# Kernel optimization log

Measured on AMD Instinct MI355X. Metric: run time of the kernel, lower is better.

## Reference

```python
import jax, jax.numpy as jnp
import numpy as np

N = 100000
E = 1600000
E_PAIR = 100000
D_IN = 128
D_H = 128


def _sage_mean(x, src, dst, W_neigh, W_self, b):
    # DGL SAGEConv('mean'): out = fc_self(h_dst) + fc_neigh(mean_{u in N(v)} h_u) + bias
    n = x.shape[0]
    msg_sum = jax.ops.segment_sum(x[src], dst, num_segments=n)          # [N, d]
    deg = jax.ops.segment_sum(jnp.ones(src.shape, x.dtype), dst, num_segments=n)
    h_neigh = msg_sum / jnp.maximum(deg, 1.0)[:, None]
    return x @ W_self.T + h_neigh @ W_neigh.T + b


def setup_inputs() -> dict:
    key = jax.random.key(0)
    ks = jax.random.split(key, 16)
    def lin(k, fan_out, fan_in):
        s = 1.0 / np.sqrt(fan_in)
        return jax.random.uniform(k, (fan_out, fan_in), jnp.float32, -s, s)
    inp = {
        'x': jax.random.normal(ks[0], (N, D_IN), jnp.float32),
        'edge_src': jax.random.randint(ks[1], (E,), 0, N),
        'edge_dst': jax.random.randint(ks[2], (E,), 0, N),
        'pos_src': jax.random.randint(ks[3], (E_PAIR,), 0, N),
        'pos_dst': jax.random.randint(ks[4], (E_PAIR,), 0, N),
        'neg_src': jax.random.randint(ks[5], (E_PAIR,), 0, N),
        'neg_dst': jax.random.randint(ks[6], (E_PAIR,), 0, N),
        # SAGEConv layer 1 (in_feats -> n_hidden)
        'W1_neigh': lin(ks[7], D_H, D_IN),
        'W1_self': lin(ks[8], D_H, D_IN),
        'b1': jnp.zeros((D_H,), jnp.float32),
        # SAGEConv layer 2 (n_hidden -> n_hidden)
        'W2_neigh': lin(ks[9], D_H, D_H),
        'W2_self': lin(ks[10], D_H, D_H),
        'b2': jnp.zeros((D_H,), jnp.float32),
        # predictor MLP: Linear(2h->h) ReLU Linear(h->h) ReLU Linear(h->1)
        'P1_w': lin(ks[11], D_H, 2 * D_H),
        'P1_b': jnp.zeros((D_H,), jnp.float32),
        'P2_w': lin(ks[12], D_H, D_H),
        'P2_b': jnp.zeros((D_H,), jnp.float32),
        'P3_w': lin(ks[13], 1, D_H),
        'P3_b': jnp.zeros((1,), jnp.float32),
    }
    return inp


def _predict(h_src, h_dst, P1_w, P1_b, P2_w, P2_b, P3_w, P3_b):
    h = jnp.concatenate([h_src, h_dst], axis=1)
    h = jax.nn.relu(h @ P1_w.T + P1_b)
    h = jax.nn.relu(h @ P2_w.T + P2_b)
    return h @ P3_w.T + P3_b


def reference(x, edge_src, edge_dst, pos_src, pos_dst, neg_src, neg_dst,
              W1_neigh, W1_self, b1, W2_neigh, W2_self, b2,
              P1_w, P1_b, P2_w, P2_b, P3_w, P3_b):
    h = _sage_mean(x, edge_src, edge_dst, W1_neigh, W1_self, b1)
    h = jax.nn.relu(h)
    h = _sage_mean(h, edge_src, edge_dst, W2_neigh, W2_self, b2)
    h_pos = _predict(h[pos_src], h[pos_dst], P1_w, P1_b, P2_w, P2_b, P3_w, P3_b)
    h_neg = _predict(h[neg_src], h[neg_dst], P1_w, P1_b, P2_w, P2_b, P3_w, P3_b)
    return (h_pos, h_neg)
```

## Files before the change

kernel.cpp:

```cpp
#include <hip/hip_runtime.h>
#include <hip/hip_bf16.h>
#include <hip/hip_fp16.h>


#define D 128
#define NR 512
#define PART_CHUNK 4096
#define LDA 40
#define LDC 264

typedef _Float16 f16x8 __attribute__((ext_vector_type(8)));
typedef float f32x4 __attribute__((ext_vector_type(4)));

__global__ __launch_bounds__(256) void k_regcount(
    const int* __restrict__ dst, int* __restrict__ region_cnt, int e, int bound) {
    __shared__ int s[NR];
    for (int i = threadIdx.x; i < NR; i += 256) s[i] = 0;
    __syncthreads();
    for (int i = blockIdx.x * 256 + threadIdx.x; i < e; i += gridDim.x * 256)
        atomicAdd(&s[dst[i] / bound], 1);
    __syncthreads();
    for (int i = threadIdx.x; i < NR; i += 256)
        if (s[i]) atomicAdd(&region_cnt[i], s[i]);
}

__global__ void k_regbase(const int* __restrict__ region_cnt,
                          int* __restrict__ region_base, int* __restrict__ region_cursor) {
    if (threadIdx.x == 0 && blockIdx.x == 0) {
        int run = 0;
        for (int r = 0; r < NR; ++r) {
            region_base[r] = run; region_cursor[r] = run; run += region_cnt[r];
        }
        region_base[NR] = run;
    }
}

__global__ __launch_bounds__(256) void k_regpart(
    const int* __restrict__ src, const int* __restrict__ dst,
    unsigned int* __restrict__ eout, int* __restrict__ region_cursor, int e, int bound) {
    __shared__ int s_cnt[NR];
    __shared__ int s_base[NR];
    for (int c0 = blockIdx.x * PART_CHUNK; c0 < e; c0 += gridDim.x * PART_CHUNK) {
        int cend = min(c0 + PART_CHUNK, e);
        for (int i = threadIdx.x; i < NR; i += 256) s_cnt[i] = 0;
        __syncthreads();
        for (int i = c0 + threadIdx.x; i < cend; i += 256)
            atomicAdd(&s_cnt[dst[i] / bound], 1);
        __syncthreads();
        for (int i = threadIdx.x; i < NR; i += 256)
            s_base[i] = s_cnt[i] ? atomicAdd(&region_cursor[i], s_cnt[i]) : 0;
        __syncthreads();
        for (int i = threadIdx.x; i < NR; i += 256) s_cnt[i] = 0;
        __syncthreads();
        for (int i = c0 + threadIdx.x; i < cend; i += 256) {
            int d = dst[i];
            int r = d / bound;
            unsigned int doff = (unsigned int)(d - r * bound);
            int p = atomicAdd(&s_cnt[r], 1);
            eout[s_base[r] + p] = (unsigned int)src[i] | (doff << 20);
        }
        __syncthreads();
    }
}

__global__ __launch_bounds__(256) void k_rowoff(
    const unsigned int* __restrict__ ep, const int* __restrict__ region_base,
    int* __restrict__ row_off, int n, int bound) {
    int r = blockIdx.x;
    int rlo = r * bound;
    if (threadIdx.x == 0 && r == 0) row_off[n] = region_base[NR];
    if (rlo >= n) return;
    int nn = min(bound, n - rlo);
    __shared__ int s_deg[256];
    __shared__ int s_scan[256];
    if (threadIdx.x < 256) s_deg[threadIdx.x] = 0;
    __syncthreads();
    int beg = region_base[r], end = region_base[r + 1];
    for (int i = beg + threadIdx.x; i < end; i += 256)
        atomicAdd(&s_deg[ep[i] >> 20], 1);
    __syncthreads();
    int v = (threadIdx.x < nn) ? s_deg[threadIdx.x] : 0;
    s_scan[threadIdx.x] = v;
    __syncthreads();
    #pragma unroll
    for (int off = 1; off < 256; off <<= 1) {
        int add = (threadIdx.x >= off) ? s_scan[threadIdx.x - off] : 0;
        __syncthreads();
        s_scan[threadIdx.x] += add;
        __syncthreads();
    }
    if (threadIdx.x < nn)
        row_off[rlo + threadIdx.x] = region_base[r] +
            (threadIdx.x ? s_scan[threadIdx.x - 1] : 0);
}

__global__ __launch_bounds__(256) void k_scatter3(
    const unsigned int* __restrict__ ep, const int* __restrict__ region_base,
    const int* __restrict__ row_off, int* __restrict__ csr, int n, int bound) {
    int r = blockIdx.x;
    int rlo = r * bound;
    if (rlo >= n) return;
    int nn = min(bound, n - rlo);
    __shared__ int s_cur[256];
    __shared__ int s_ro[256];
    if (threadIdx.x < nn) {
        s_cur[threadIdx.x] = 0;
        s_ro[threadIdx.x] = row_off[rlo + threadIdx.x];
    }
    __syncthreads();
    int beg = region_base[r], end = region_base[r + 1];
    for (int i = beg + threadIdx.x; i < end; i += 256) {
        unsigned int v = ep[i];
        int doff = v >> 20;
        int srcn = v & 0xFFFFF;
        int p = atomicAdd(&s_cur[doff], 1);
        csr[s_ro[doff] + p] = srcn;
    }
}

__global__ void k_cvt_f16(const float* __restrict__ src, _Float16* __restrict__ dst, int n8) {
    int i = blockIdx.x * 256 + threadIdx.x;
    if (i >= n8) return;
    const float4* s4 = (const float4*)src;
    float4 a = s4[2 * i], b = s4[2 * i + 1];
    f16x8 h;
    h[0] = (_Float16)a.x; h[1] = (_Float16)a.y; h[2] = (_Float16)a.z; h[3] = (_Float16)a.w;
    h[4] = (_Float16)b.x; h[5] = (_Float16)b.y; h[6] = (_Float16)b.z; h[7] = (_Float16)b.w;
    *(f16x8*)(dst + 8 * i) = h;
}

__global__ void k_cvt_weights(
    const float* __restrict__ W1s, const float* __restrict__ W1n,
    const float* __restrict__ W2s, const float* __restrict__ W2n,
    const float* __restrict__ P1w, const float* __restrict__ P2w,
    _Float16* __restrict__ Ws1f, _Float16* __restrict__ Wn1f,
    _Float16* __restrict__ Ws2f, _Float16* __restrict__ Wn2f,
    _Float16* __restrict__ P1wf, _Float16* __restrict__ P2wf) {
    int g = blockIdx.x * 256 + threadIdx.x;
    const float* src; _Float16* dst; int off;
    if      (g <  2048) { src = W1s; dst = Ws1f; off = g; }
    else if (g <  4096) { src = W1n; dst = Wn1f; off = g - 2048; }
    else if (g <  6144) { src = W2s; dst = Ws2f; off = g - 4096; }
    else if (g <  8192) { src = W2n; dst = Wn2f; off = g - 6144; }
    else if (g < 12288) { src = P1w; dst = P1wf; off = g - 8192; }
    else if (g < 14336) { src = P2w; dst = P2wf; off = g - 12288; }
    else return;
    const float4* s4 = (const float4*)src;
    float4 a = s4[2 * off], b = s4[2 * off + 1];
    f16x8 h;
    h[0] = (_Float16)a.x; h[1] = (_Float16)a.y; h[2] = (_Float16)a.z; h[3] = (_Float16)a.w;
    h[4] = (_Float16)b.x; h[5] = (_Float16)b.y; h[6] = (_Float16)b.z; h[7] = (_Float16)b.w;
    *(f16x8*)(dst + 8 * off) = h;
}

__global__ __launch_bounds__(256) void k_agg(
    const _Float16* __restrict__ Xf, const int* __restrict__ row_off,
    const int* __restrict__ csr, _Float16* __restrict__ Aggf, int n_nodes) {
    int g = blockIdx.x * 16 + (threadIdx.x >> 4);
    if (g >= n_nodes) return;
    int l = threadIdx.x & 15;
    int beg = row_off[g], end = row_off[g + 1];
    float acc[8] = {0.f, 0.f, 0.f, 0.f, 0.f, 0.f, 0.f, 0.f};
    int i = beg;
    for (; i + 4 <= end; i += 4) {
        int s0 = csr[i], s1 = csr[i + 1], s2 = csr[i + 2], s3 = csr[i + 3];
        f16x8 v0 = *(const f16x8*)(Xf + (size_t)s0 * D + l * 8);
        f16x8 v1 = *(const f16x8*)(Xf + (size_t)s1 * D + l * 8);
        f16x8 v2 = *(const f16x8*)(Xf + (size_t)s2 * D + l * 8);
        f16x8 v3 = *(const f16x8*)(Xf + (size_t)s3 * D + l * 8);
        #pragma unroll
        for (int j = 0; j < 8; ++j)
            acc[j] += ((float)v0[j] + (float)v1[j]) + ((float)v2[j] + (float)v3[j]);
    }
    for (; i < end; ++i) {
        int s0 = csr[i];
        f16x8 v0 = *(const f16x8*)(Xf + (size_t)s0 * D + l * 8);
        #pragma unroll
        for (int j = 0; j < 8; ++j) acc[j] += (float)v0[j];
    }
    float inv = 1.0f / fmaxf((float)(end - beg), 1.0f);
    f16x8 o;
    #pragma unroll
    for (int j = 0; j < 8; ++j) o[j] = (_Float16)(acc[j] * inv);
    *(f16x8*)(Aggf + (size_t)g * D + l * 8) = o;
}

__global__ __launch_bounds__(512) void k_transform(
    const _Float16* __restrict__ Xf, const _Float16* __restrict__ Aggf,
    const _Float16* __restrict__ Wsf, const _Float16* __restrict__ Wnf,
    const float* __restrict__ bias, _Float16* __restrict__ outf,
    int n_rows, int do_relu) {
    __shared__ _Float16 s_a[2][128 * LDA];
    __shared__ _Float16 s_b[2][128 * LDA];
    int tid = threadIdx.x;
    int w = tid >> 6, l = tid & 63;
    int wr = w >> 1, wc = w & 1;
    int l15 = l & 15, lk = l >> 4;
    int n0 = blockIdx.x * 128;
    int r = tid >> 2, q = tid & 3;
    int rstage = n0 + r; if (rstage >= n_rows) rstage = n_rows - 1;

    f32x4 acc[2][4];
    #pragma unroll
    for (int i = 0; i < 2; ++i)
        #pragma unroll
        for (int j = 0; j < 4; ++j) acc[i][j] = (f32x4){0.f, 0.f, 0.f, 0.f};

    int a_off = (wr * 32 + l15) * LDA + lk * 8;
    int b_off = (wc * 64 + l15) * LDA + lk * 8;
    int st_off = r * LDA + q * 8;

    {
        f16x8 av = *(const f16x8*)(Xf + (size_t)rstage * D + q * 8);
        f16x8 wv = *(const f16x8*)(Wsf + (size_t)r * D + q * 8);
        *(f16x8*)(&s_a[0][st_off]) = av;
        *(f16x8*)(&s_b[0][st_off]) = wv;
    }
    __syncthreads();

    for (int c = 0; c < 8; ++c) {
        int b = c & 1;
        f16x8 av, wv;
        if (c < 7) {
            int cn = c + 1;
            const _Float16* asrc = (cn < 4) ? Xf : Aggf;
            const _Float16* wsrc = (cn < 4) ? Wsf : Wnf;
            int kb = (cn & 3) * 32;
            av = *(const f16x8*)(asrc + (size_t)rstage * D + kb + q * 8);
            wv = *(const f16x8*)(wsrc + (size_t)r * D + kb + q * 8);
        }
        f16x8 af[2], bf[4];
        af[0] = *(const f16x8*)(&s_a[b][a_off]);
        af[1] = *(const f16x8*)(&s_a[b][a_off + 16 * LDA]);
        #pragma unroll
        for (int j = 0; j < 4; ++j) bf[j] = *(const f16x8*)(&s_b[b][b_off + j * 16 * LDA]);
        #pragma unroll
        for (int i = 0; i < 2; ++i)
            #pragma unroll
            for (int j = 0; j < 4; ++j)
                acc[i][j] = __builtin_amdgcn_mfma_f32_16x16x32_f16(af[i], bf[j], acc[i][j], 0, 0, 0);
        if (c < 7) {
            *(f16x8*)(&s_a[b ^ 1][st_off]) = av;
            *(f16x8*)(&s_b[b ^ 1][st_off]) = wv;
        }
        __syncthreads();
    }

    #pragma unroll
    for (int j = 0; j < 4; ++j) {
        int col = wc * 64 + j * 16 + l15;
        float bv = bias[col];
        #pragma unroll
        for (int i = 0; i < 2; ++i) {
            int rowb = n0 + wr * 32 + i * 16 + lk * 4;
            #pragma unroll
            for (int v = 0; v < 4; ++v) {
                int row = rowb + v;
                if (row < n_rows) {
                    float xv = acc[i][j][v] + bv;
                    if (do_relu) xv = fmaxf(xv, 0.f);
                    outf[(size_t)row * D + col] = (_Float16)xv;
                }
            }
        }
    }
}

__global__ __launch_bounds__(256) void k_mlp(
    const _Float16* __restrict__ Hf,
    const int* __restrict__ pos_src, const int* __restrict__ pos_dst,
    const int* __restrict__ neg_src, const int* __restrict__ neg_dst,
    const _Float16* __restrict__ P1wf, const float* __restrict__ P1b,
    const _Float16* __restrict__ P2wf, const float* __restrict__ P2b,
    const float* __restrict__ P3w, const float* __restrict__ P3b,
    float* __restrict__ out, int EP) {
    __shared__ _Float16 s_cat[64 * LDC];
    __shared__ _Float16 s_b[2][128 * LDA];
    __shared__ float s_red[64 * 2];
    __shared__ int s_node[128];
    int tid = threadIdx.x;
    int w = tid >> 6, l = tid & 63;
    int wr = w >> 1, wc = w & 1;
    int l15 = l & 15, lk = l >> 4;
    int p0 = blockIdx.x * 64;
    int twoEP = 2 * EP;

    if (tid < 128) {
        int p = p0 + (tid & 63);
        if (p >= twoEP) p = twoEP - 1;
        int node;
        if (tid < 64) node = (p < EP) ? pos_src[p] : neg_src[p - EP];
        else          node = (p < EP) ? pos_dst[p] : neg_dst[p - EP];
        s_node[tid] = node;
    }
    __syncthreads();

    #pragma unroll
    for (int e = 0; e < 8; ++e) {
        int idx = tid + e * 256;
        int rr = idx >> 4, u = idx & 15;
        int node = s_node[rr];
        f16x8 v = *(const f16x8*)(Hf + (size_t)node * D + u * 8);
        *(f16x8*)(s_cat + (rr & 63) * LDC + (rr >> 6) * 128 + u * 8) = v;
    }
    #pragma unroll
    for (int e = 0; e < 2; ++e) {
        int idx = tid + e * 256;
        int o = idx >> 2, q = idx & 3;
        *(f16x8*)(&s_b[0][o * LDA + q * 8]) = *(const f16x8*)(P1wf + (size_t)o * 256 + q * 8);
    }
    __syncthreads();

    f32x4 acc[2][4];
    #pragma unroll
    for (int i = 0; i < 2; ++i)
        #pragma unroll
        for (int j = 0; j < 4; ++j) acc[i][j] = (f32x4){0.f, 0.f, 0.f, 0.f};

    for (int c = 0; c < 8; ++c) {
        int b = c & 1;
        f16x8 nw[2];
        if (c < 7) {
            #pragma unroll
            for (int e = 0; e < 2; ++e) {
                int idx = tid + e * 256;
                int o = idx >> 2, q = idx & 3;
                nw[e] = *(const f16x8*)(P1wf + (size_t)o * 256 + (c + 1) * 32 + q * 8);
            }
        }
        f16x8 af[2], bf[4];
        af[0] = *(const f16x8*)(s_cat + (wr * 32 + l15) * LDC + c * 32 + lk * 8);
        af[1] = *(const f16x8*)(s_cat + (wr * 32 + 16 + l15) * LDC + c * 32 + lk * 8);
        #pragma unroll
        for (int j = 0; j < 4; ++j)
            bf[j] = *(const f16x8*)(&s_b[b][(wc * 64 + j * 16 + l15) * LDA + lk * 8]);
        #pragma unroll
        for (int i = 0; i < 2; ++i)
            #pragma unroll
            for (int j = 0; j < 4; ++j)
                acc[i][j] = __builtin_amdgcn_mfma_f32_16x16x32_f16(af[i], bf[j], acc[i][j], 0, 0, 0);
        if (c < 7) {
            #pragma unroll
            for (int e = 0; e < 2; ++e) {
                int idx = tid + e * 256;
                int o = idx >> 2, q = idx & 3;
                *(f16x8*)(&s_b[b ^ 1][o * LDA + q * 8]) = nw[e];
            }
        }
        __syncthreads();
    }

    #pragma unroll
    for (int j = 0; j < 4; ++j) {
        int col = wc * 64 + j * 16 + l15;
        float bv = P1b[col];
        #pragma unroll
        for (int i = 0; i < 2; ++i) {
            int rowb = wr * 32 + i * 16 + lk * 4;
            #pragma unroll
            for (int v = 0; v < 4; ++v)
                s_cat[(rowb + v) * LDC + col] = (_Float16)fmaxf(acc[i][j][v] + bv, 0.f);
        }
    }
    #pragma unroll
    for (int e = 0; e < 2; ++e) {
        int idx = tid + e * 256;
        int o = idx >> 2, q = idx & 3;
        *(f16x8*)(&s_b[0][o * LDA + q * 8]) = *(const f16x8*)(P2wf + (size_t)o * D + q * 8);
    }
    __syncthreads();

    f32x4 acc2[2][4];
    #pragma unroll
    for (int i = 0; i < 2; ++i)
        #pragma unroll
        for (int j = 0; j < 4; ++j) acc2[i][j] = (f32x4){0.f, 0.f, 0.f, 0.f};

    for (int c = 0; c < 4; ++c) {
        int b = c & 1;
        f16x8 nw[2];
        if (c < 3) {
            #pragma unroll
            for (int e = 0; e < 2; ++e) {
                int idx = tid + e * 256;
                int o = idx >> 2, q = idx & 3;
                nw[e] = *(const f16x8*)(P2wf + (size_t)o * D + (c + 1) * 32 + q * 8);
            }
        }
        f16x8 af[2], bf[4];
        af[0] = *(const f16x8*)(s_cat + (wr * 32 + l15) * LDC + c * 32 + lk * 8);
        af[1] = *(const f16x8*)(s_cat + (wr * 32 + 16 + l15) * LDC + c * 32 + lk * 8);
        #pragma unroll
        for (int j = 0; j < 4; ++j)
            bf[j] = *(const f16x8*)(&s_b[b][(wc * 64 + j * 16 + l15) * LDA + lk * 8]);
        #pragma unroll
        for (int i = 0; i < 2; ++i)
            #pragma unroll
            for (int j = 0; j < 4; ++j)
                acc2[i][j] = __builtin_amdgcn_mfma_f32_16x16x32_f16(af[i], bf[j], acc2[i][j], 0, 0, 0);
        if (c < 3) {
            #pragma unroll
            for (int e = 0; e < 2; ++e) {
                int idx = tid + e * 256;
                int o = idx >> 2, q = idx & 3;
                *(f16x8*)(&s_b[b ^ 1][o * LDA + q * 8]) = nw[e];
            }
        }
        __syncthreads();
    }

    float b2v[4], pw[4];
    #pragma unroll
    for (int j = 0; j < 4; ++j) {
        int col = wc * 64 + j * 16 + l15;
        b2v[j] = P2b[col];
        pw[j] = P3w[col];
    }
    #pragma unroll
    for (int i = 0; i < 2; ++i) {
        #pragma unroll
        for (int v = 0; v < 4; ++v) {
            float s = 0.f;
            #pragma unroll
            for (int j = 0; j < 4; ++j)
                s += fmaxf(acc2[i][j][v] + b2v[j], 0.f) * pw[j];
            s += __shfl_xor(s, 1);
            s += __shfl_xor(s, 2);
            s += __shfl_xor(s, 4);
            s += __shfl_xor(s, 8);
            if (l15 == 0)
                s_red[(wr * 32 + i * 16 + lk * 4 + v) * 2 + wc] = s;
        }
    }
    __syncthreads();
    if (tid < 64) {
        int p = p0 + tid;
        if (p < twoEP) out[p] = s_red[tid * 2] + s_red[tid * 2 + 1] + P3b[0];
    }
}

static inline size_t align_up(size_t x, size_t a) { return (x + a - 1) & ~(a - 1); }

extern "C" void kernel_launch(void* const* d_in, const int* in_sizes, int n_in,
                              void* d_out, int out_size, void* d_ws, size_t ws_size,
                              hipStream_t stream) {
    const float* x        = (const float*)d_in[0];
    const int*   edge_src = (const int*)d_in[1];
    const int*   edge_dst = (const int*)d_in[2];
    const int*   pos_src  = (const int*)d_in[3];
    const int*   pos_dst  = (const int*)d_in[4];
    const int*   neg_src  = (const int*)d_in[5];
    const int*   neg_dst  = (const int*)d_in[6];
    const float* W1n = (const float*)d_in[7];
    const float* W1s = (const float*)d_in[8];
    const float* b1  = (const float*)d_in[9];
    const float* W2n = (const float*)d_in[10];
    const float* W2s = (const float*)d_in[11];
    const float* b2  = (const float*)d_in[12];
    const float* P1w = (const float*)d_in[13];
    const float* P1b = (const float*)d_in[14];
    const float* P2w = (const float*)d_in[15];
    const float* P2b = (const float*)d_in[16];
    const float* P3w = (const float*)d_in[17];
    const float* P3b = (const float*)d_in[18];
    float* out = (float*)d_out;

    const int N = in_sizes[0] / D;
    const int E = in_sizes[1];
    const int EP = in_sizes[3];
    const int bound = (N + NR - 1) / NR;

    char* ws = (char*)d_ws;
    size_t off = 0;
    int* row_off = (int*)(ws + off); off = align_up(off + (size_t)(N + 1) * 4, 256);
    int* regmeta = (int*)(ws + off); off = align_up(off + (size_t)(3 * NR + 8) * 4, 256);
    int* csr     = (int*)(ws + off); off = align_up(off + (size_t)E * 4, 256);
    unsigned int* epart = (unsigned int*)(ws + off); off = align_up(off + (size_t)E * 4, 256);
    _Float16* xf   = (_Float16*)(ws + off); off = align_up(off + (size_t)N * D * 2, 256);
    _Float16* aggf = (_Float16*)(ws + off); off = align_up(off + (size_t)N * D * 2, 256);
    _Float16* h1f  = (_Float16*)(ws + off); off = align_up(off + (size_t)N * D * 2, 256);
    _Float16* h2f  = (_Float16*)(ws + off); off = align_up(off + (size_t)N * D * 2, 256);
    _Float16* Ws1f = (_Float16*)(ws + off); off = align_up(off + (size_t)D * D * 2, 256);
    _Float16* Wn1f = (_Float16*)(ws + off); off = align_up(off + (size_t)D * D * 2, 256);
    _Float16* Ws2f = (_Float16*)(ws + off); off = align_up(off + (size_t)D * D * 2, 256);
    _Float16* Wn2f = (_Float16*)(ws + off); off = align_up(off + (size_t)D * D * 2, 256);
    _Float16* P1wf = (_Float16*)(ws + off); off = align_up(off + (size_t)2 * D * D * 2, 256);
    _Float16* P2wf = (_Float16*)(ws + off); off = align_up(off + (size_t)D * D * 2, 256);
    (void)ws_size;

    int* region_cnt    = regmeta;
    int* region_base   = regmeta + NR;
    int* region_cursor = regmeta + 2 * NR + 4;

    hipMemsetAsync(region_cnt, 0, NR * 4, stream);
    k_regcount<<<128, 256, 0, stream>>>(edge_dst, region_cnt, E, bound);
    k_regbase<<<1, 1, 0, stream>>>(region_cnt, region_base, region_cursor);
    k_regpart<<<(E + PART_CHUNK - 1) / PART_CHUNK, 256, 0, stream>>>(
        edge_src, edge_dst, epart, region_cursor, E, bound);
    k_rowoff<<<NR, 256, 0, stream>>>(epart, region_base, row_off, N, bound);
    k_scatter3<<<NR, 256, 0, stream>>>(epart, region_base, row_off, csr, N, bound);

    k_cvt_f16<<<(N * D / 8 + 255) / 256, 256, 0, stream>>>(x, xf, N * D / 8);
    k_cvt_weights<<<56, 256, 0, stream>>>(W1s, W1n, W2s, W2n, P1w, P2w,
                                          Ws1f, Wn1f, Ws2f, Wn2f, P1wf, P2wf);

    const int ngrid = (N + 127) / 128;
    const int pgrid = (2 * EP + 63) / 64;

    k_agg<<<(N + 15) / 16, 256, 0, stream>>>(xf, row_off, csr, aggf, N);
    k_transform<<<ngrid, 512, 0, stream>>>(xf, aggf, Ws1f, Wn1f, b1, h1f, N, 1);
    k_agg<<<(N + 15) / 16, 256, 0, stream>>>(h1f, row_off, csr, aggf, N);
    k_transform<<<ngrid, 512, 0, stream>>>(h1f, aggf, Ws2f, Wn2f, b2, h2f, N, 0);

    k_mlp<<<pgrid, 256, 0, stream>>>(h2f, pos_src, pos_dst, neg_src, neg_dst,
                                     P1wf, P1b, P2wf, P2b, P3w, P3b, out, EP);
}
```

Before: 326.4 us.

## Precompute per-node predictor first-layer projections before gathering edge pairs

Splits the first predictor linear layer into source and destination halves and applies each once per node in a new GEMM kernel, k_pre. That kernel writes an N×256 half-precision table, which reuses the xf buffer and spills into the adjacent aggf buffer. The pair MLP then gathers the two precomputed halves, adds the bias and applies ReLU, which removes the per-pair 256-wide GEMM. It trades roughly half the first-layer FLOPs for an extra kernel launch and a large intermediate that must be written and then gathered.

```diff
diff --git a/kernel.cpp b/kernel.cpp
--- a/kernel.cpp
+++ b/kernel.cpp
@@ -7,7 +7,7 @@
 #define NR 512
 #define PART_CHUNK 4096
 #define LDA 40
-#define LDC 264
+#define LDH2 136
 
 typedef _Float16 f16x8 __attribute__((ext_vector_type(8)));
 typedef float f32x4 __attribute__((ext_vector_type(4)));
@@ -135,16 +135,26 @@
     const float* __restrict__ P1w, const float* __restrict__ P2w,
     _Float16* __restrict__ Ws1f, _Float16* __restrict__ Wn1f,
     _Float16* __restrict__ Ws2f, _Float16* __restrict__ Wn2f,
-    _Float16* __restrict__ P1wf, _Float16* __restrict__ P2wf) {
+    _Float16* __restrict__ P1cf, _Float16* __restrict__ P2wf) {
     int g = blockIdx.x * 256 + threadIdx.x;
+    if (g >= 14336) return;
     const float* src; _Float16* dst; int off;
+    if (g >= 8192 && g < 12288) {
+        int u = g - 8192;
+        int o = u >> 4, col = (u & 15) * 8;
+        src = P1w + (size_t)(o & 127) * 256 + ((o >> 7) * 128) + col;
+        float4 a = *(const float4*)src, b = *(const float4*)(src + 4);
+        f16x8 h;
+        h[0] = (_Float16)a.x; h[1] = (_Float16)a.y; h[2] = (_Float16)a.z; h[3] = (_Float16)a.w;
+        h[4] = (_Float16)b.x; h[5] = (_Float16)b.y; h[6] = (_Float16)b.z; h[7] = (_Float16)b.w;
+        *(f16x8*)(P1cf + (size_t)u * 8) = h;
+        return;
+    }
     if      (g <  2048) { src = W1s; dst = Ws1f; off = g; }
     else if (g <  4096) { src = W1n; dst = Wn1f; off = g - 2048; }
     else if (g <  6144) { src = W2s; dst = Ws2f; off = g - 4096; }
     else if (g <  8192) { src = W2n; dst = Wn2f; off = g - 6144; }
-    else if (g < 12288) { src = P1w; dst = P1wf; off = g - 8192; }
-    else if (g < 14336) { src = P2w; dst = P2wf; off = g - 12288; }
-    else return;
+    else                { src = P2w; dst = P2wf; off = g - 12288; }
     const float4* s4 = (const float4*)src;
     float4 a = s4[2 * off], b = s4[2 * off + 1];
     f16x8 h;
@@ -266,15 +276,80 @@
     }
 }
 
+__global__ __launch_bounds__(512) void k_pre(
+    const _Float16* __restrict__ Hf, const _Float16* __restrict__ P1cf,
+    _Float16* __restrict__ Pre, int n_rows) {
+    __shared__ _Float16 s_a[64 * LDA];
+    __shared__ _Float16 s_b[256 * LDA];
+    int tid = threadIdx.x;
+    int w = tid >> 6, l = tid & 63;
+    int wr = w >> 2, wc = w & 3;
+    int l15 = l & 15, lk = l >> 4;
+    int n0 = blockIdx.x * 64;
+
+    f32x4 acc[2][4];
+    #pragma unroll
+    for (int i = 0; i < 2; ++i)
+        #pragma unroll
+        for (int j = 0; j < 4; ++j) acc[i][j] = (f32x4){0.f, 0.f, 0.f, 0.f};
+
+    int a_off = (wr * 32 + l15) * LDA + lk * 8;
+
+    for (int c = 0; c < 4; ++c) {
+        int kb = c * 32;
+        __syncthreads();
+        if (tid < 256) {
+            int r = tid >> 2, q = tid & 3;
+            int rstage = n0 + r; if (rstage >= n_rows) rstage = n_rows - 1;
+            *(f16x8*)(&s_a[r * LDA + q * 8]) =
+                *(const f16x8*)(Hf + (size_t)rstage * D + kb + q * 8);
+        }
+        #pragma unroll
+        for (int e = 0; e < 2; ++e) {
+            int idx = tid + e * 512;
+            int o = idx >> 2, q = idx & 3;
+            *(f16x8*)(&s_b[o * LDA + q * 8]) =
+                *(const f16x8*)(P1cf + (size_t)o * 128 + kb + q * 8);
+        }
+        __syncthreads();
+        f16x8 af[2], bf[4];
+        af[0] = *(const f16x8*)(&s_a[a_off]);
+        af[1] = *(const f16x8*)(&s_a[a_off + 16 * LDA]);
+        #pragma unroll
+        for (int j = 0; j < 4; ++j)
+            bf[j] = *(const f16x8*)(&s_b[(wc * 64 + j * 16 + l15) * LDA + lk * 8]);
+        #pragma unroll
+        for (int i = 0; i < 2; ++i)
+            #pragma unroll
+            for (int j = 0; j < 4; ++j)
+                acc[i][j] = __builtin_amdgcn_mfma_f32_16x16x32_f16(af[i], bf[j], acc[i][j], 0, 0, 0);
+    }
+
+    #pragma unroll
+    for (int j = 0; j < 4; ++j) {
+        int col = wc * 64 + j * 16 + l15;
+        #pragma unroll
+        for (int i = 0; i < 2; ++i) {
+            int rowb = n0 + wr * 32 + i * 16 + lk * 4;
+            #pragma unroll
+            for (int v = 0; v < 4; ++v) {
+                int row = rowb + v;
+                if (row < n_rows)
+                    Pre[(size_t)row * 256 + col] = (_Float16)acc[i][j][v];
+            }
+        }
+    }
+}
+
 __global__ __launch_bounds__(256) void k_mlp(
-    const _Float16* __restrict__ Hf,
+    const _Float16* __restrict__ Pre,
     const int* __restrict__ pos_src, const int* __restrict__ pos_dst,
     const int* __restrict__ neg_src, const int* __restrict__ neg_dst,
-    const _Float16* __restrict__ P1wf, const float* __restrict__ P1b,
+    const float* __restrict__ P1b,
     const _Float16* __restrict__ P2wf, const float* __restrict__ P2b,
     const float* __restrict__ P3w, const float* __restrict__ P3b,
     float* __restrict__ out, int EP) {
-    __shared__ _Float16 s_cat[64 * LDC];
+    __shared__ _Float16 s_h1[64 * LDH2];
     __shared__ _Float16 s_b[2][128 * LDA];
     __shared__ float s_red[64 * 2];
     __shared__ int s_node[128];
@@ -296,71 +371,20 @@
     __syncthreads();
 
     #pragma unroll
-    for (int e = 0; e < 8; ++e) {
+    for (int e = 0; e < 4; ++e) {
         int idx = tid + e * 256;
-        int rr = idx >> 4, u = idx & 15;
-        int node = s_node[rr];
-        f16x8 v = *(const f16x8*)(Hf + (size_t)node * D + u * 8);
-        *(f16x8*)(s_cat + (rr & 63) * LDC + (rr >> 6) * 128 + u * 8) = v;
-    }
-    #pragma unroll
-    for (int e = 0; e < 2; ++e) {
-        int idx = tid + e * 256;
-        int o = idx >> 2, q = idx & 3;
-        *(f16x8*)(&s_b[0][o * LDA + q * 8]) = *(const f16x8*)(P1wf + (size_t)o * 256 + q * 8);
-    }
-    __syncthreads();
-
-    f32x4 acc[2][4];
-    #pragma unroll
-    for (int i = 0; i < 2; ++i)
-        #pragma unroll
-        for (int j = 0; j < 4; ++j) acc[i][j] = (f32x4){0.f, 0.f, 0.f, 0.f};
-
-    for (int c = 0; c < 8; ++c) {
-        int b = c & 1;
-        f16x8 nw[2];
-        if (c < 7) {
-            #pragma unroll
-            for (int e = 0; e < 2; ++e) {
-                int idx = tid + e * 256;
-                int o = idx >> 2, q = idx & 3;
-                nw[e] = *(const f16x8*)(P1wf + (size_t)o * 256 + (c + 1) * 32 + q * 8);
-            }
-        }
-        f16x8 af[2], bf[4];
-        af[0] = *(const f16x8*)(s_cat + (wr * 32 + l15) * LDC + c * 32 + lk * 8);
-        af[1] = *(const f16x8*)(s_cat + (wr * 32 + 16 + l15) * LDC + c * 32 + lk * 8);
-        #pragma unroll
-        for (int j = 0; j < 4; ++j)
-            bf[j] = *(const f16x8*)(&s_b[b][(wc * 64 + j * 16 + l15) * LDA + lk * 8]);
-        #pragma unroll
-        for (int i = 0; i < 2; ++i)
-            #pragma unroll
-            for (int j = 0; j < 4; ++j)
-                acc[i][j] = __builtin_amdgcn_mfma_f32_16x16x32_f16(af[i], bf[j], acc[i][j], 0, 0, 0);
-        if (c < 7) {
-            #pragma unroll
-            for (int e = 0; e < 2; ++e) {
-                int idx = tid + e * 256;
-                int o = idx >> 2, q = idx & 3;
-                *(f16x8*)(&s_b[b ^ 1][o * LDA + q * 8]) = nw[e];
-            }
-        }
-        __syncthreads();
-    }
-
-    #pragma unroll
-    for (int j = 0; j < 4; ++j) {
-        int col = wc * 64 + j * 16 + l15;
-        float bv = P1b[col];
-        #pragma unroll
-        for (int i = 0; i < 2; ++i) {
-            int rowb = wr * 32 + i * 16 + lk * 4;
-            #pragma unroll
-            for (int v = 0; v < 4; ++v)
-                s_cat[(rowb + v) * LDC + col] = (_Float16)fmaxf(acc[i][j][v] + bv, 0.f);
-        }
+        int pr = idx >> 4, u = idx & 15;
+        int sn = s_node[pr], dn = s_node[64 + pr];
+        f16x8 a = *(const f16x8*)(Pre + (size_t)sn * 256 + u * 8);
+        f16x8 b = *(const f16x8*)(Pre + (size_t)dn * 256 + 128 + u * 8);
+        float4 b0 = *(const float4*)(P1b + u * 8);
+        float4 b1 = *(const float4*)(P1b + u * 8 + 4);
+        float bb[8] = {b0.x, b0.y, b0.z, b0.w, b1.x, b1.y, b1.z, b1.w};
+        f16x8 h;
+        #pragma unroll
+        for (int j = 0; j < 8; ++j)
+            h[j] = (_Float16)fmaxf((float)a[j] + (float)b[j] + bb[j], 0.f);
+        *(f16x8*)(&s_h1[pr * LDH2 + u * 8]) = h;
     }
     #pragma unroll
     for (int e = 0; e < 2; ++e) {
@@ -388,8 +412,8 @@
             }
         }
         f16x8 af[2], bf[4];
-        af[0] = *(const f16x8*)(s_cat + (wr * 32 + l15) * LDC + c * 32 + lk * 8);
-        af[1] = *(const f16x8*)(s_cat + (wr * 32 + 16 + l15) * LDC + c * 32 + lk * 8);
+        af[0] = *(const f16x8*)(&s_h1[(wr * 32 + l15) * LDH2 + c * 32 + lk * 8]);
+        af[1] = *(const f16x8*)(&s_h1[(wr * 32 + 16 + l15) * LDH2 + c * 32 + lk * 8]);
         #pragma unroll
         for (int j = 0; j < 4; ++j)
             bf[j] = *(const f16x8*)(&s_b[b][(wc * 64 + j * 16 + l15) * LDA + lk * 8]);
@@ -484,9 +508,11 @@
     _Float16* Wn1f = (_Float16*)(ws + off); off = align_up(off + (size_t)D * D * 2, 256);
     _Float16* Ws2f = (_Float16*)(ws + off); off = align_up(off + (size_t)D * D * 2, 256);
     _Float16* Wn2f = (_Float16*)(ws + off); off = align_up(off + (size_t)D * D * 2, 256);
-    _Float16* P1wf = (_Float16*)(ws + off); off = align_up(off + (size_t)2 * D * D * 2, 256);
+    _Float16* P1cf = (_Float16*)(ws + off); off = align_up(off + (size_t)2 * D * D * 2, 256);
     _Float16* P2wf = (_Float16*)(ws + off); off = align_up(off + (size_t)D * D * 2, 256);
     (void)ws_size;
+
+    _Float16* Pre = xf;
 
     int* region_cnt    = regmeta;
     int* region_base   = regmeta + NR;
@@ -502,7 +528,7 @@
 
     k_cvt_f16<<<(N * D / 8 + 255) / 256, 256, 0, stream>>>(x, xf, N * D / 8);
     k_cvt_weights<<<56, 256, 0, stream>>>(W1s, W1n, W2s, W2n, P1w, P2w,
-                                          Ws1f, Wn1f, Ws2f, Wn2f, P1wf, P2wf);
+                                          Ws1f, Wn1f, Ws2f, Wn2f, P1cf, P2wf);
 
     const int ngrid = (N + 127) / 128;
     const int pgrid = (2 * EP + 63) / 64;
@@ -512,6 +538,7 @@
     k_agg<<<(N + 15) / 16, 256, 0, stream>>>(h1f, row_off, csr, aggf, N);
     k_transform<<<ngrid, 512, 0, stream>>>(h1f, aggf, Ws2f, Wn2f, b2, h2f, N, 0);
 
-    k_mlp<<<pgrid, 256, 0, stream>>>(h2f, pos_src, pos_dst, neg_src, neg_dst,
-                                     P1wf, P1b, P2wf, P2b, P3w, P3b, out, EP);
-}
+    k_pre<<<(N + 63) / 64, 512, 0, stream>>>(h2f, P1cf, Pre, N);
+    k_mlp<<<pgrid, 256, 0, stream>>>(Pre, pos_src, pos_dst, neg_src, neg_dst,
+                                     P1b, P2wf, P2b, P3w, P3b, out, EP);
+}
```

Result: faster. 317.2 us (-2.8%).
